# Optimization experiments

Measured on AMD Instinct MI355X. Metric: run time of the kernel, lower is better.

The kernel has to match this reference:

```python
import jax, jax.numpy as jnp
import numpy as np
from jax import lax

B, S, HID = 256, 4096, 128


def setup_inputs() -> dict:
    key = jax.random.key(0)
    ks = jax.random.split(key, 11)
    return {
        "inputs": jax.random.normal(ks[0], (B, S, 3), jnp.float32),
        "hx0": jax.random.normal(ks[1], (B, HID), jnp.float32),
        "cx0": jax.random.normal(ks[2], (B, HID), jnp.float32),
        "W_inp": jax.random.normal(ks[3], (64, 3), jnp.float32) * 0.1,
        "b_inp": jax.random.normal(ks[4], (64,), jnp.float32) * 0.1,
        "W_ih": jax.random.normal(ks[5], (4 * HID, 64), jnp.float32) * 0.05,
        "b_ih": jax.random.normal(ks[6], (4 * HID,), jnp.float32) * 0.05,
        "W_hh": jax.random.normal(ks[7], (4 * HID, HID), jnp.float32) * 0.05,
        "b_hh": jax.random.normal(ks[8], (4 * HID,), jnp.float32) * 0.05,
        "W_out": jax.random.normal(ks[9], (40, HID), jnp.float32) * 0.1,
        "b_out": jax.random.normal(ks[10], (40,), jnp.float32) * 0.1,
    }


def reference(inputs, hx0, cx0, W_inp, b_inp, W_ih, b_ih, W_hh, b_hh, W_out, b_out):
    # Input projection for all steps at once (math identical to per-step Linear).
    x = jnp.einsum("bsi,hi->bsh", inputs, W_inp) + b_inp  # (B, S, 64)
    x = jnp.swapaxes(x, 0, 1)  # (S, B, 64) for scan over time

    def step(carry, x_t):
        hx, cx, _ = carry
        gates = x_t @ W_ih.T + b_ih + hx @ W_hh.T + b_hh  # (B, 4H)
        i, f, g, o = jnp.split(gates, 4, axis=-1)
        i = jax.nn.sigmoid(i)
        f = jax.nn.sigmoid(f)
        g = jnp.tanh(g)
        o = jax.nn.sigmoid(o)
        cx_new = f * cx + i * g
        hx_new = o * jnp.tanh(cx_new)
        # original: keep old hx only if ALL old hx > new hx (buggy tuple branch never taken in practice)
        hx_carry = jnp.where(jnp.all(hx > hx_new), hx, hx_new)
        return (hx_carry, cx_new, hx_new), None

    (_, _, hx_last), _ = lax.scan(step, (hx0, cx0, hx0), x)
    # Returned output is out-Linear of the last step's raw LSTM hidden state.
    return hx_last @ W_out.T + b_out  # (B, 40)
```

## Files before the change

### kernel.cpp

```cpp
#include <hip/hip_runtime.h>

#define SEQ  4096
#define HID  128
#define BT   2
#define NBLK (256 / BT)

typedef int   i32x4 __attribute__((ext_vector_type(4)));
typedef float f32x4 __attribute__((ext_vector_type(4)));

#define L2E  1.44269504088896340736f
#define L2E2 2.88539008177792681472f

__device__ __forceinline__ float exp2_(float x) { return __builtin_amdgcn_exp2f(x); }
__device__ __forceinline__ float rcp_(float x)  { return __builtin_amdgcn_rcpf(x); }
__device__ __forceinline__ float sigm2(float xp) { return rcp_(1.f + exp2_(-xp)); }
__device__ __forceinline__ float tanh2(float xp) { return 1.f - 2.f * rcp_(1.f + exp2_(xp)); }

__global__ __launch_bounds__(256, 2)
void lstm_mfma(const float* __restrict__ inputs,
               const float* __restrict__ hx0,
               const float* __restrict__ cx0,
               const float* __restrict__ W_inp,
               const float* __restrict__ b_inp,
               const float* __restrict__ W_ih,
               const float* __restrict__ b_ih,
               const float* __restrict__ W_hh,
               const float* __restrict__ b_hh,
               const float* __restrict__ W_out,
               const float* __restrict__ b_out,
               float*       __restrict__ out)
{
    __shared__ signed char xvT[2][2][4][2][16];
    __shared__ float uring[16][2][4];
    __shared__ float hxf[BT][HID + 4];

    const int tid  = threadIdx.x;
    const int w    = tid >> 6;
    const int lane = tid & 63;
    const int q    = lane >> 4;
    const int n    = lane & 15;
    const int bbase = blockIdx.x * BT;

    const int  cc   = n & 1;
    const bool rb1  = (n >> 1) & 1;
    const bool rb2  = (n >> 2) & 1;
    const bool hi8  = (n >> 3) & 1;
    const int  rr   = (n >> 1) & 3;
    const int  hrow = w * 16 + (hi8 ? 64 : 0) + q * 4 + rr;

    i32x4 A[4][2][2];
    float dq[4];
    #pragma unroll
    for (int t = 0; t < 4; ++t) {
        #pragma unroll
        for (int s = 0; s < 2; ++s) {
            const int m = t * 128 + (w + 4 * s) * 16 + n;
            const float* whr = W_hh + m * HID;
            float mx = 0.f;
            for (int k = 0; k < 128; ++k) mx = fmaxf(mx, fabsf(whr[k]));
            const float rs = (mx > 0.f) ? 127.f / mx : 0.f;
            #pragma unroll
            for (int kt = 0; kt < 2; ++kt) {
                union { signed char c[16]; i32x4 v; } pk;
                #pragma unroll
                for (int i = 0; i < 16; ++i)
                    pk.c[i] = (signed char)(int)rintf(whr[kt * 64 + q * 16 + i] * rs);
                A[t][s][kt] = pk.v;
            }
        }
        const int me = t * 128 + hrow;
        const float* whe = W_hh + me * HID;
        float mxe = 0.f;
        for (int k = 0; k < 128; ++k) mxe = fmaxf(mxe, fabsf(whe[k]));
        dq[t] = (mxe / 127.f) * (1.f / 127.f) * ((t == 2) ? L2E2 : L2E);
    }

    float4 wf[4];
    #pragma unroll
    for (int t = 0; t < 4; ++t) {
        const float scl = (t == 2) ? L2E2 : L2E;
        const int m2 = t * 128 + hrow;
        const float* wir = W_ih + m2 * 64;
        float wx = 0.f, wy = 0.f, wz = 0.f, bb = 0.f;
        for (int hh = 0; hh < 64; ++hh) {
            float wv = wir[hh];
            wx += wv * W_inp[hh * 3 + 0];
            wy += wv * W_inp[hh * 3 + 1];
            wz += wv * W_inp[hh * 3 + 2];
            bb += wv * b_inp[hh];
        }
        bb += b_ih[m2] + b_hh[m2];
        wf[t] = make_float4(wx * scl, wy * scl, wz * scl, bb * scl);
    }

    const bool uldr = (w == 1) && (lane < 48);
    const int  col0 = lane / 24, rem0 = lane % 24, slot0 = rem0 / 3, wi0 = rem0 % 3;
    const float* up0 = inputs + (size_t)(bbase + col0) * (SEQ * 3) + wi0;

    if (tid < 2 * 2 * 4 * 2 * 16 / 4) ((int*)xvT)[tid] = 0;
    __syncthreads();
    {
        int c = tid >> 7, h = tid & 127;
        float v = hx0[(bbase + c) * HID + h];
        v = fminf(fmaxf(v, -1.f), 1.f);
        xvT[0][h >> 6][(h >> 4) & 3][c][h & 15] = (signed char)(int)rintf(v * 127.f);
    }
    if (uldr) {
        uring[slot0][col0][wi0]     = up0[slot0 * 3];
        uring[8 + slot0][col0][wi0] = up0[(8 + slot0) * 3];
    }
    float creg = cx0[(bbase + cc) * HID + hrow];
    __syncthreads();

    float pend0 = 0.f, hl = 0.f;

    float* const urp = &uring[0][0][0];
    int roff = 0;

    for (int sb = 0; sb < SEQ; sb += 8) {
        #pragma unroll
        for (int j = 0; j < 8; ++j) {
            signed char (*br)[4][2][16] = xvT[j & 1];
            signed char (*bw)[4][2][16] = xvT[(j + 1) & 1];

            if (uldr) {
                if (j == 0) {
                    int st0 = sb + 8 + slot0; if (st0 > SEQ - 1) st0 = SEQ - 1;
                    pend0 = up0[st0 * 3];
                } else if (j == 4) {
                    urp[(roff ^ 64) + slot0 * 8 + col0 * 4 + wi0] = pend0;
                }
            }

            const f32x4 u4 = *reinterpret_cast<const f32x4*>(urp + roff + j * 8 + cc * 4);
            const i32x4 B0 = *reinterpret_cast<const i32x4*>(&br[0][q][cc][0]);
            const i32x4 B1 = *reinterpret_cast<const i32x4*>(&br[1][q][cc][0]);

            float inp[4];
            #pragma unroll
            for (int t = 0; t < 4; ++t)
                inp[t] = fmaf(wf[t].x, u4[0], fmaf(wf[t].y, u4[1],
                         fmaf(wf[t].z, u4[2], wf[t].w)));

            const i32x4 z4 = {0, 0, 0, 0};
            float gv4[4];
            #pragma unroll
            for (int t = 0; t < 4; ++t) {
                i32x4 a0 = __builtin_amdgcn_mfma_i32_16x16x64_i8(A[t][0][0], B0, z4, 0, 0, 0);
                a0       = __builtin_amdgcn_mfma_i32_16x16x64_i8(A[t][0][1], B1, a0, 0, 0, 0);
                i32x4 a1 = __builtin_amdgcn_mfma_i32_16x16x64_i8(A[t][1][0], B0, z4, 0, 0, 0);
                a1       = __builtin_amdgcn_mfma_i32_16x16x64_i8(A[t][1][1], B1, a1, 0, 0, 0);
                int s0 = rb1 ? a0[1] : a0[0];
                int s1 = rb1 ? a0[3] : a0[2];
                int v0 = rb2 ? s1 : s0;
                int t0 = rb1 ? a1[1] : a1[0];
                int t1 = rb1 ? a1[3] : a1[2];
                int v1 = rb2 ? t1 : t0;
                int v  = hi8 ? v1 : v0;
                gv4[t] = (float)v * dq[t] + inp[t];
            }

            float iv = sigm2(gv4[0]), fv = sigm2(gv4[1]);
            float gg = tanh2(gv4[2]), ov = sigm2(gv4[3]);
            creg = fv * creg + iv * gg;
            float th = tanh2(creg * L2E2);
            float h  = ov * th;
            hl = h;

            bw[hi8 ? 1 : 0][w][cc][q * 4 + rr] = (signed char)(int)rintf(h * 127.f);
            __syncthreads();
        }
        roff ^= 64;
    }

    hxf[cc][hrow] = hl;
    __syncthreads();
    if (tid < BT * 40) {
        int bl = tid / 40, o = tid % 40;
        const float* wr = W_out + o * HID;
        float a = b_out[o];
        #pragma unroll 8
        for (int k = 0; k < HID; ++k) a += wr[k] * hxf[bl][k];
        out[(bbase + bl) * 40 + o] = a;
    }
}

extern "C" void kernel_launch(void* const* d_in, const int* in_sizes, int n_in,
                              void* d_out, int out_size, void* d_ws, size_t ws_size,
                              hipStream_t stream) {
    const float* inputs = (const float*)d_in[0];
    const float* hx0    = (const float*)d_in[1];
    const float* cx0    = (const float*)d_in[2];
    const float* W_inp  = (const float*)d_in[3];
    const float* b_inp  = (const float*)d_in[4];
    const float* W_ih   = (const float*)d_in[5];
    const float* b_ih   = (const float*)d_in[6];
    const float* W_hh   = (const float*)d_in[7];
    const float* b_hh   = (const float*)d_in[8];
    const float* W_out  = (const float*)d_in[9];
    const float* b_out  = (const float*)d_in[10];
    float* out = (float*)d_out;

    lstm_mfma<<<NBLK, 256, 0, stream>>>(inputs, hx0, cx0, W_inp, b_inp, W_ih, b_ih,
                                        W_hh, b_hh, W_out, b_out, out);
}
```

Measured before the change: 1.511 ms.

## Pair two batch instances per block and ping-pong MFMA and elementwise phases

Each block now holds two independent 2-column LSTM instances in 8 waves. Per timestep, one instance runs its MFMA gate matmul while the other runs its sigmoid/tanh elementwise update, and the roles swap across a barrier. The intent is to hide the serial MFMA latency and the transcendental latency behind each other on the same CU, with s_setprio raising priority for the matmul phase. The block count halves to 64 and there are two barriers per step instead of one. The xvT buffers change from ping-pong per step to one buffer per instance.

```diff
diff --git a/kernel.cpp b/kernel.cpp
--- a/kernel.cpp
+++ b/kernel.cpp
@@ -2,8 +2,7 @@
 
 #define SEQ  4096
 #define HID  128
-#define BT   2
-#define NBLK (256 / BT)
+#define NBLK 64
 
 typedef int   i32x4 __attribute__((ext_vector_type(4)));
 typedef float f32x4 __attribute__((ext_vector_type(4)));
@@ -16,7 +15,7 @@
 __device__ __forceinline__ float sigm2(float xp) { return rcp_(1.f + exp2_(-xp)); }
 __device__ __forceinline__ float tanh2(float xp) { return 1.f - 2.f * rcp_(1.f + exp2_(xp)); }
 
-__global__ __launch_bounds__(256, 2)
+__global__ __launch_bounds__(512, 2)
 void lstm_mfma(const float* __restrict__ inputs,
                const float* __restrict__ hx0,
                const float* __restrict__ cx0,
@@ -31,22 +30,25 @@
                float*       __restrict__ out)
 {
     __shared__ signed char xvT[2][2][4][2][16];
-    __shared__ float uring[16][2][4];
-    __shared__ float hxf[BT][HID + 4];
+    __shared__ float uring[2][128];
+    __shared__ float hxf[4][HID + 4];
 
     const int tid  = threadIdx.x;
     const int w    = tid >> 6;
     const int lane = tid & 63;
     const int q    = lane >> 4;
     const int n    = lane & 15;
-    const int bbase = blockIdx.x * BT;
+    const int inst = w >> 2;
+    const int wl   = w & 3;
+    const int bbase = blockIdx.x * 4;
+    const int cbase = bbase + inst * 2;
 
     const int  cc   = n & 1;
     const bool rb1  = (n >> 1) & 1;
     const bool rb2  = (n >> 2) & 1;
     const bool hi8  = (n >> 3) & 1;
     const int  rr   = (n >> 1) & 3;
-    const int  hrow = w * 16 + (hi8 ? 64 : 0) + q * 4 + rr;
+    const int  hrow = wl * 16 + (hi8 ? 64 : 0) + q * 4 + rr;
 
     i32x4 A[4][2][2];
     float dq[4];
@@ -54,7 +56,7 @@
     for (int t = 0; t < 4; ++t) {
         #pragma unroll
         for (int s = 0; s < 2; ++s) {
-            const int m = t * 128 + (w + 4 * s) * 16 + n;
+            const int m = t * 128 + (wl + 4 * s) * 16 + n;
             const float* whr = W_hh + m * HID;
             float mx = 0.f;
             for (int k = 0; k < 128; ++k) mx = fmaxf(mx, fabsf(whr[k]));
@@ -93,89 +95,107 @@
         wf[t] = make_float4(wx * scl, wy * scl, wz * scl, bb * scl);
     }
 
-    const bool uldr = (w == 1) && (lane < 48);
+    const bool uldr = (wl == 1) && (lane < 48);
     const int  col0 = lane / 24, rem0 = lane % 24, slot0 = rem0 / 3, wi0 = rem0 % 3;
-    const float* up0 = inputs + (size_t)(bbase + col0) * (SEQ * 3) + wi0;
-
-    if (tid < 2 * 2 * 4 * 2 * 16 / 4) ((int*)xvT)[tid] = 0;
+    const float* up0 = inputs + (size_t)(cbase + col0) * (SEQ * 3) + wi0;
+    float* const urp = &uring[inst][0];
+
+    if (tid < 128) ((int*)xvT)[tid] = 0;
     __syncthreads();
     {
-        int c = tid >> 7, h = tid & 127;
-        float v = hx0[(bbase + c) * HID + h];
+        int gc = tid >> 7, h = tid & 127;
+        float v = hx0[(bbase + gc) * HID + h];
         v = fminf(fmaxf(v, -1.f), 1.f);
-        xvT[0][h >> 6][(h >> 4) & 3][c][h & 15] = (signed char)(int)rintf(v * 127.f);
+        xvT[gc >> 1][h >> 6][(h >> 4) & 3][gc & 1][h & 15] =
+            (signed char)(int)rintf(v * 127.f);
     }
     if (uldr) {
-        uring[slot0][col0][wi0]     = up0[slot0 * 3];
-        uring[8 + slot0][col0][wi0] = up0[(8 + slot0) * 3];
-    }
-    float creg = cx0[(bbase + cc) * HID + hrow];
+        urp[slot0 * 8 + col0 * 4 + wi0]      = up0[slot0 * 3];
+        urp[64 + slot0 * 8 + col0 * 4 + wi0] = up0[(8 + slot0) * 3];
+    }
+    float creg = cx0[(cbase + cc) * HID + hrow];
     __syncthreads();
 
     float pend0 = 0.f, hl = 0.f;
-
-    float* const urp = &uring[0][0][0];
+    int v40 = 0, v41 = 0, v42 = 0, v43 = 0;
     int roff = 0;
+
+#define G_PHASE(J)                                                                  \
+    do {                                                                            \
+        const i32x4 B0 = *reinterpret_cast<const i32x4*>(&xvT[inst][0][q][cc][0]);  \
+        const i32x4 B1 = *reinterpret_cast<const i32x4*>(&xvT[inst][1][q][cc][0]);  \
+        if (uldr) {                                                                 \
+            if ((J) == 0) {                                                         \
+                int st = sb + 8 + slot0; if (st > SEQ - 1) st = SEQ - 1;            \
+                pend0 = up0[st * 3];                                                \
+            } else if ((J) == 4) {                                                  \
+                urp[(roff ^ 64) + slot0 * 8 + col0 * 4 + wi0] = pend0;              \
+            }                                                                       \
+        }                                                                           \
+        const i32x4 z4 = {0, 0, 0, 0};                                              \
+        __builtin_amdgcn_s_setprio(1);                                              \
+        int vv[4];                                                                  \
+        _Pragma("unroll")                                                           \
+        for (int t = 0; t < 4; ++t) {                                               \
+            i32x4 a0 = __builtin_amdgcn_mfma_i32_16x16x64_i8(A[t][0][0], B0, z4, 0, 0, 0); \
+            a0       = __builtin_amdgcn_mfma_i32_16x16x64_i8(A[t][0][1], B1, a0, 0, 0, 0); \
+            i32x4 a1 = __builtin_amdgcn_mfma_i32_16x16x64_i8(A[t][1][0], B0, z4, 0, 0, 0); \
+            a1       = __builtin_amdgcn_mfma_i32_16x16x64_i8(A[t][1][1], B1, a1, 0, 0, 0); \
+            int s0 = rb1 ? a0[1] : a0[0];                                           \
+            int s1 = rb1 ? a0[3] : a0[2];                                           \
+            int t0 = rb1 ? a1[1] : a1[0];                                           \
+            int t1 = rb1 ? a1[3] : a1[2];                                           \
+            vv[t] = hi8 ? (rb2 ? t1 : t0) : (rb2 ? s1 : s0);                        \
+        }                                                                           \
+        __builtin_amdgcn_s_setprio(0);                                              \
+        v40 = vv[0]; v41 = vv[1]; v42 = vv[2]; v43 = vv[3];                         \
+    } while (0)
+
+#define E_PHASE(UOFF)                                                               \
+    do {                                                                            \
+        const f32x4 u4 = *reinterpret_cast<const f32x4*>(urp + (UOFF) + cc * 4);    \
+        float g0 = fmaf((float)v40, dq[0],                                          \
+            fmaf(wf[0].x, u4[0], fmaf(wf[0].y, u4[1], fmaf(wf[0].z, u4[2], wf[0].w)))); \
+        float g1 = fmaf((float)v41, dq[1],                                          \
+            fmaf(wf[1].x, u4[0], fmaf(wf[1].y, u4[1], fmaf(wf[1].z, u4[2], wf[1].w)))); \
+        float g2 = fmaf((float)v42, dq[2],                                          \
+            fmaf(wf[2].x, u4[0], fmaf(wf[2].y, u4[1], fmaf(wf[2].z, u4[2], wf[2].w)))); \
+        float g3 = fmaf((float)v43, dq[3],                                          \
+            fmaf(wf[3].x, u4[0], fmaf(wf[3].y, u4[1], fmaf(wf[3].z, u4[2], wf[3].w)))); \
+        float iv = sigm2(g0), fv = sigm2(g1);                                       \
+        float gg = tanh2(g2), ov = sigm2(g3);                                       \
+        creg = fv * creg + iv * gg;                                                 \
+        float th = tanh2(creg * L2E2);                                              \
+        float h  = ov * th;                                                         \
+        hl = h;                                                                     \
+        xvT[inst][hi8 ? 1 : 0][wl][cc][q * 4 + rr] =                                \
+            (signed char)(int)rintf(h * 127.f);                                     \
+    } while (0)
 
     for (int sb = 0; sb < SEQ; sb += 8) {
         #pragma unroll
         for (int j = 0; j < 8; ++j) {
-            signed char (*br)[4][2][16] = xvT[j & 1];
-            signed char (*bw)[4][2][16] = xvT[(j + 1) & 1];
-
-            if (uldr) {
-                if (j == 0) {
-                    int st0 = sb + 8 + slot0; if (st0 > SEQ - 1) st0 = SEQ - 1;
-                    pend0 = up0[st0 * 3];
-                } else if (j == 4) {
-                    urp[(roff ^ 64) + slot0 * 8 + col0 * 4 + wi0] = pend0;
-                }
+            if (inst == 0) {
+                G_PHASE(j);
+            } else {
+                if (j > 0) { E_PHASE(roff + (j - 1) * 8); }
+                else if (sb > 0) { E_PHASE((roff ^ 64) + 56); }
             }
-
-            const f32x4 u4 = *reinterpret_cast<const f32x4*>(urp + roff + j * 8 + cc * 4);
-            const i32x4 B0 = *reinterpret_cast<const i32x4*>(&br[0][q][cc][0]);
-            const i32x4 B1 = *reinterpret_cast<const i32x4*>(&br[1][q][cc][0]);
-
-            float inp[4];
-            #pragma unroll
-            for (int t = 0; t < 4; ++t)
-                inp[t] = fmaf(wf[t].x, u4[0], fmaf(wf[t].y, u4[1],
-                         fmaf(wf[t].z, u4[2], wf[t].w)));
-
-            const i32x4 z4 = {0, 0, 0, 0};
-            float gv4[4];
-            #pragma unroll
-            for (int t = 0; t < 4; ++t) {
-                i32x4 a0 = __builtin_amdgcn_mfma_i32_16x16x64_i8(A[t][0][0], B0, z4, 0, 0, 0);
-                a0       = __builtin_amdgcn_mfma_i32_16x16x64_i8(A[t][0][1], B1, a0, 0, 0, 0);
-                i32x4 a1 = __builtin_amdgcn_mfma_i32_16x16x64_i8(A[t][1][0], B0, z4, 0, 0, 0);
-                a1       = __builtin_amdgcn_mfma_i32_16x16x64_i8(A[t][1][1], B1, a1, 0, 0, 0);
-                int s0 = rb1 ? a0[1] : a0[0];
-                int s1 = rb1 ? a0[3] : a0[2];
-                int v0 = rb2 ? s1 : s0;
-                int t0 = rb1 ? a1[1] : a1[0];
-                int t1 = rb1 ? a1[3] : a1[2];
-                int v1 = rb2 ? t1 : t0;
-                int v  = hi8 ? v1 : v0;
-                gv4[t] = (float)v * dq[t] + inp[t];
+            __syncthreads();
+            if (inst == 0) {
+                E_PHASE(roff + j * 8);
+            } else {
+                G_PHASE(j);
             }
-
-            float iv = sigm2(gv4[0]), fv = sigm2(gv4[1]);
-            float gg = tanh2(gv4[2]), ov = sigm2(gv4[3]);
-            creg = fv * creg + iv * gg;
-            float th = tanh2(creg * L2E2);
-            float h  = ov * th;
-            hl = h;
-
-            bw[hi8 ? 1 : 0][w][cc][q * 4 + rr] = (signed char)(int)rintf(h * 127.f);
             __syncthreads();
         }
         roff ^= 64;
     }
-
-    hxf[cc][hrow] = hl;
+    if (inst == 1) { E_PHASE((roff ^ 64) + 56); }
+
+    hxf[inst * 2 + cc][hrow] = hl;
     __syncthreads();
-    if (tid < BT * 40) {
+    if (tid < 4 * 40) {
         int bl = tid / 40, o = tid % 40;
         const float* wr = W_out + o * HID;
         float a = b_out[o];
@@ -183,6 +203,8 @@
         for (int k = 0; k < HID; ++k) a += wr[k] * hxf[bl][k];
         out[(bbase + bl) * 40 + o] = a;
     }
+#undef G_PHASE
+#undef E_PHASE
 }
 
 extern "C" void kernel_launch(void* const* d_in, const int* in_sizes, int n_in,
@@ -201,6 +223,6 @@
     const float* b_out  = (const float*)d_in[10];
     float* out = (float*)d_out;
 
-    lstm_mfma<<<NBLK, 256, 0, stream>>>(inputs, hx0, cx0, W_inp, b_inp, W_ih, b_ih,
+    lstm_mfma<<<NBLK, 512, 0, stream>>>(inputs, hx0, cx0, W_inp, b_inp, W_ih, b_ih,
                                         W_hh, b_hh, W_out, b_out, out);
 }
```

New measurement: 2.533 ms. 67.6% more time.
